# Optimization experiments

Hardware: AMD Instinct MI355X
Metric: run time of the kernel (lower is better)

The kernel has to match this reference:

```python
import jax, jax.numpy as jnp
import numpy as np

N = 50000        # num_nodes
E = 800000       # num edges (avg degree 16)
IN = 512         # embedding_dim[0]
H = 128          # hidden_dim = embedding_dim[1]
C = 64           # out_dim = n_classes = embedding_dim[-1]
L = 3            # layer_num = len(embedding_dim) - 1


def _lin(k, fan_in, fan_out):
    s = 1.0 / np.sqrt(fan_in)
    k1, k2 = jax.random.split(k)
    W = jax.random.uniform(k1, (fan_in, fan_out), jnp.float32, -s, s)
    b = jax.random.uniform(k2, (fan_out,), jnp.float32, -s, s)
    return W, b


def setup_inputs() -> dict:
    key = jax.random.key(0)
    ks = jax.random.split(key, 12)
    d = {}
    d["x"] = jax.random.normal(ks[0], (N, IN), jnp.float32)
    d["edge_index"] = jax.random.randint(ks[1], (2, E), 0, N)
    # pseudo_mlp: in_dim -> 512 -> 64 -> out_dim
    d["Wp1"], d["bp1"] = _lin(ks[2], IN, 512)
    d["Wp2"], d["bp2"] = _lin(ks[3], 512, 64)
    d["Wp3"], d["bp3"] = _lin(ks[4], 64, C)
    # parsing_mats[0] (only ln=0 is used in learn_soft_edge3), init ones/scaling_factor
    d["parsing0"] = jnp.ones((C, C), jnp.float32) / 2.0 + 0.01 * jax.random.normal(ks[5], (C, C), jnp.float32)
    # GCNConv weights (PyG style: linear without bias, bias added after aggregation)
    d["Wg0"], d["bg0"] = _lin(ks[6], IN, H)
    d["Wg1"], d["bg1"] = _lin(ks[7], H, H)
    d["Wg2"], d["bg2"] = _lin(ks[8], H, H)
    # JK 'cat' -> lin1 input is (layer_num-1)*hidden
    d["Wl1"], d["bl1"] = _lin(ks[9], (L - 1) * H, H)
    d["Wl2"], d["bl2"] = _lin(ks[10], H, C)
    return d


def gcn_conv(x, W, b, edge_index, ew, n):
    """PyG GCNConv with per-edge weight ew, add_self_loops=True (loop weight 1)."""
    xw = x @ W                                           # [N, F_out]
    row, col = edge_index[0], edge_index[1]
    loop = jnp.arange(n)
    row2 = jnp.concatenate([row, loop])
    col2 = jnp.concatenate([col, loop])
    ew2 = jnp.concatenate([ew, jnp.ones((n,), xw.dtype)])
    deg = jax.ops.segment_sum(ew2, col2, num_segments=n)
    dis = jnp.where(deg > 0, jax.lax.rsqrt(deg), 0.0)    # deg^-1/2, inf -> 0
    norm = dis[row2] * ew2 * dis[col2]                   # [E+N]
    out = jax.ops.segment_sum(norm[:, None] * xw[row2], col2, num_segments=n)
    return out + b


def soft_edge_weight(x, edge_index, Wp1, bp1, Wp2, bp2, Wp3, bp3, parsing0):
    """learn_soft_edge3: bilinear form start^T * relu(2*P) * end per edge.
    Original materializes an [E,C,C] outer product then bmm + diagonal; the
    diagonal-sum equals einsum('ek,ed,dk->e', start, end, parsing), computed
    here as a fused small matmul + elementwise reduce (same math)."""
    h = jax.nn.relu(x @ Wp1 + bp1)
    h = jax.nn.relu(h @ Wp2 + bp2)
    logits = h @ Wp3 + bp3                               # [N, C]
    parsing = jax.nn.relu(2.0 * parsing0)                # scaling_factor = 2
    s = logits[edge_index[0]]                            # [E, C] start
    e = logits[edge_index[1]]                            # [E, C] end
    ew = jnp.sum((e @ parsing) * s, axis=-1)             # [E]
    mean = ew.mean()
    var = jnp.var(ew, ddof=1)                            # torch .var() is unbiased
    return (ew - mean) * jnp.sqrt(1e-4 / var) + 1.0


def reference(x, edge_index, Wp1, bp1, Wp2, bp2, Wp3, bp3, parsing0,
              Wg0, bg0, Wg1, bg1, Wg2, bg2, Wl1, bl1, Wl2, bl2):
    n = x.shape[0]
    ew = soft_edge_weight(x, edge_index, Wp1, bp1, Wp2, bp2, Wp3, bp3, parsing0)
    # layer 0
    x1 = jax.nn.relu(gcn_conv(x, Wg0, bg0, edge_index, ew, n))
    xs = [x1]
    # ln = 1 (not last): conv -> relu -> (dropout off in eval) -> append
    x2 = jax.nn.relu(gcn_conv(x1, Wg1, bg1, edge_index, ew, n))
    xs.append(x2)
    # ln = 2 (last layer): computed in original but loop breaks before append;
    # jump(xs) overwrites x, so the last conv's output never reaches the output.
    xj = jnp.concatenate(xs, axis=-1)                    # JK 'cat' -> [N, (L-1)*H]
    out = jax.nn.relu(xj @ Wl1 + bl1)
    out = out @ Wl2 + bl2                                # [N, C]
    return out
```

## Files before the change

### kernel.cpp

```cpp
#include <hip/hip_runtime.h>
#include <hip/hip_bf16.h>
#include <cmath>
#include <cstring>

#define NNODES 50000
#define NEDGES 800000
#define IND    512
#define HD     128
#define CD     64

typedef __bf16 bf16x8 __attribute__((ext_vector_type(8)));
typedef float  f32x4  __attribute__((ext_vector_type(4)));
typedef const __attribute__((address_space(1))) unsigned int* gu32p;
typedef __attribute__((address_space(3))) unsigned int* lu32p;

static const size_t XJ_B   = 0;
static const size_t HID_B  = 25600000;
static const size_t H1_B   = 51200000;
static const size_t XW_B   = 102400000;
static const size_t H2_B   = 115200000;
static const size_t LG_B   = 121600000;
static const size_t PE_B   = 128000000;
static const size_t WT_B   = 134400000;
static const size_t CSRR_B = 135300000;
static const size_t EWC_B  = 138500000;
static const size_t CSRW_B = 141700000;
static const size_t CNT_B  = 144900000;
static const size_t S_B    = 145100000;
static const size_t ZERO_BYTES = 200016;
static const size_t RP_B   = 145100016;
static const size_t WOFF_B = 145300020;
static const size_t INCL_B = 145500020;
static const size_t BSUM_B = 145700020;
static const size_t ST_B   = 145701044;
static const size_t DIS_B  = 145701052;

static const size_t WP1T_O = 0;
static const size_t WG0T_O = 524288;
static const size_t WP2T_O = 655360;
static const size_t WP3T_O = 720896;
static const size_t W2T_O  = 729088;
static const size_t WG1T_O = 737280;
static const size_t WL1T_O = 770048;
static const size_t WL2T_O = 835584;
static const size_t BG1_O  = 851968;
static const size_t BG3_O  = 854528;

struct WD { const float* s; __hip_bfloat16* d; int K; int N; };
struct PrepArgs {
    const float* x; __hip_bfloat16* xb;
    WD w[7];
    int bo[8];
    const float* Wp3; const float* bp3; const float* P0; const float* bp1;
    __hip_bfloat16* W2t; float* bias_g1; float* bias_g3;
};
#define PREP_CAST_BLKS 12500
#define PREP_TP_BLKS   1648
#define PREP_BLKS      (PREP_CAST_BLKS + PREP_TP_BLKS + 20)

__global__ __launch_bounds__(256) void prep_all(PrepArgs a)
{
    int b = blockIdx.x;
    int t = threadIdx.x;
    if (b < PREP_CAST_BLKS) {
        int i = b * 256 + t;
        const float4* p = (const float4*)a.x + (size_t)i * 2;
        float4 u = p[0], v = p[1];
        __hip_bfloat16 o[8] __attribute__((aligned(16)));
        o[0] = __float2bfloat16(u.x); o[1] = __float2bfloat16(u.y);
        o[2] = __float2bfloat16(u.z); o[3] = __float2bfloat16(u.w);
        o[4] = __float2bfloat16(v.x); o[5] = __float2bfloat16(v.y);
        o[6] = __float2bfloat16(v.z); o[7] = __float2bfloat16(v.w);
        *(int4*)(a.xb + (size_t)i * 8) = *(const int4*)o;
        return;
    }
    b -= PREP_CAST_BLKS;
    if (b < PREP_TP_BLKS) {
        int m = 0;
        #pragma unroll
        for (int q = 1; q < 7; q++) if (b >= a.bo[q]) m = q;
        WD d = a.w[m];
        int i = (b - a.bo[m]) * 256 + t;
        if (i < d.K * d.N) {
            int k = i % d.K, n = i / d.K;
            d.d[i] = __float2bfloat16(d.s[(size_t)k * d.N + n]);
        }
        return;
    }
    b -= PREP_TP_BLKS;
    if (b < 16) {
        int i = b * 256 + t;
        int k = i >> 6, n = i & 63;
        float s = 0.f;
        for (int j = 0; j < 64; j++)
            s += a.Wp3[k * 64 + j] * fmaxf(2.f * a.P0[j * 64 + n], 0.f);
        a.W2t[n * 64 + k] = __float2bfloat16(s);
    } else if (b == 16) {
        int n = t;
        if (n < 64) {
            float s = 0.f;
            for (int j = 0; j < 64; j++)
                s += a.bp3[j] * fmaxf(2.f * a.P0[j * 64 + n], 0.f);
            a.bias_g3[n] = a.bp3[n];
            a.bias_g3[64 + n] = s;
        }
    } else {
        int i = (b - 17) * 256 + t;
        if (i < 512) a.bias_g1[i] = a.bp1[i];
        else if (i < 640) a.bias_g1[i] = 0.f;
    }
}

template<int BM, int BN, int WN>
__global__ __launch_bounds__(256) void gemm_mfma(
    const __hip_bfloat16* __restrict__ Ab, int lda,
    const __hip_bfloat16* __restrict__ Bt, int ldb,
    const float* __restrict__ bias,
    void* __restrict__ Cout, int ldc,
    void* __restrict__ Cout2, int ldc2, int splitN,
    int M, int K, int do_relu, int out_bf16)
{
    constexpr int BF = WN / 16;
    constexpr int MI = BM / 32;
    constexpr int APASS = BM / 64;
    constexpr int BPASS = BN / 64;
    __shared__ __bf16 As[2][BM * 32];
    __shared__ __bf16 Bs[2][BN * 32];

    const int NC = gridDim.x, NR = gridDim.y;
    int g = blockIdx.y * NC + blockIdx.x;
    int per = NC * 8;
    int nfull = (NR >> 3) * per;
    int rowt, colt;
    if (g < nfull) {
        int grp = g / per, rem = g % per;
        rowt = grp * 8 + (rem & 7);
        colt = rem >> 3;
    } else {
        int rem = g - nfull;
        int tail = NR - (NR >> 3) * 8;
        rowt = (NR >> 3) * 8 + rem % tail;
        colt = rem / tail;
    }

    const int t = threadIdx.x;
    const int row0 = rowt * BM;
    const int col0 = colt * BN;

    const int wv   = t >> 6;
    const int lane = t & 63;
    const int quad = lane >> 4;
    const int l16  = lane & 15;
    const int wrow = (wv >> 1) * (BM / 2);
    const int wcol = (wv & 1) * WN;

    const int subrow = lane >> 2;
    const int kchunk = (lane & 3) ^ (subrow & 3);
    const int subkg  = kchunk * 8;

    f32x4 acc[MI][BF] = {};

    for (int k0 = 0; k0 < K; k0 += 64) {
        #pragma unroll
        for (int h = 0; h < 2; h++) {
            int kh = k0 + h * 32;
            #pragma unroll
            for (int p = 0; p < APASS; p++) {
                int rowA = (p * 4 + wv) * 16 + subrow;
                const __hip_bfloat16* gp = Ab + (size_t)(row0 + rowA) * lda + kh + subkg;
                __builtin_amdgcn_global_load_lds((gu32p)(const void*)gp,
                    (lu32p)(void*)&As[h][(p * 4 + wv) * 512], 16, 0, 0);
            }
            #pragma unroll
            for (int p = 0; p < BPASS; p++) {
                int rowB = (p * 4 + wv) * 16 + subrow;
                const __hip_bfloat16* gp = Bt + (size_t)(col0 + rowB) * ldb + kh + subkg;
                __builtin_amdgcn_global_load_lds((gu32p)(const void*)gp,
                    (lu32p)(void*)&Bs[h][(p * 4 + wv) * 512], 16, 0, 0);
            }
        }
        __syncthreads();

        #pragma unroll
        for (int h = 0; h < 2; h++) {
            bf16x8 af[MI], bfr[BF];
            #pragma unroll
            for (int i = 0; i < MI; i++) {
                int R = wrow + i * 16 + l16;
                af[i] = *(const bf16x8*)&As[h][R * 32 + ((quad ^ (R & 3)) * 8)];
            }
            #pragma unroll
            for (int j = 0; j < BF; j++) {
                int R = wcol + j * 16 + l16;
                bfr[j] = *(const bf16x8*)&Bs[h][R * 32 + ((quad ^ (R & 3)) * 8)];
            }
            #pragma unroll
            for (int i = 0; i < MI; i++)
                #pragma unroll
                for (int j = 0; j < BF; j++)
                    acc[i][j] = __builtin_amdgcn_mfma_f32_16x16x32_bf16(af[i], bfr[j], acc[i][j], 0, 0, 0);
        }
        if (k0 + 64 < K) __syncthreads();
    }

    #pragma unroll
    for (int i = 0; i < MI; i++) {
        #pragma unroll
        for (int j = 0; j < BF; j++) {
            int n = col0 + wcol + j * 16 + l16;
            bool second = (n >= splitN);
            float bv = bias ? bias[n] : 0.f;
            #pragma unroll
            for (int reg = 0; reg < 4; reg++) {
                int m = row0 + wrow + i * 16 + quad * 4 + reg;
                if (m >= M) continue;
                float v = acc[i][j][reg] + bv;
                if (do_relu && !second) v = fmaxf(v, 0.f);
                if (second)
                    ((__hip_bfloat16*)Cout2)[(size_t)m * ldc2 + (n - splitN)] = __float2bfloat16(v);
                else if (out_bf16)
                    ((__hip_bfloat16*)Cout)[(size_t)m * ldc + n] = __float2bfloat16(v);
                else
                    ((float*)Cout)[(size_t)m * ldc + n] = v;
            }
        }
    }
}

__global__ __launch_bounds__(256) void count_kernel(
    const int* __restrict__ ei, int* __restrict__ cnt)
{
    int e = blockIdx.x * 256 + threadIdx.x;
    if (e >= NEDGES) return;
    atomicAdd(&cnt[ei[NEDGES + e]], 1);
}

__global__ __launch_bounds__(256) void scan1_kernel(
    const int* __restrict__ cnt, int* __restrict__ incl, int* __restrict__ bsum)
{
    __shared__ int s[256];
    int t = threadIdx.x;
    int i = blockIdx.x * 256 + t;
    int v = (i < NNODES) ? cnt[i] : 0;
    s[t] = v;
    __syncthreads();
    for (int off = 1; off < 256; off <<= 1) {
        int u = (t >= off) ? s[t - off] : 0;
        __syncthreads();
        s[t] += u;
        __syncthreads();
    }
    if (i < NNODES) incl[i] = s[t];
    if (t == 255) bsum[blockIdx.x] = s[255];
}

__global__ __launch_bounds__(256) void scan3_kernel(
    const int* __restrict__ cnt, const int* __restrict__ incl,
    const int* __restrict__ bsum, int* __restrict__ rowptr,
    int* __restrict__ woff, int nb)
{
    __shared__ int s[256];
    int t = threadIdx.x;
    int v = (t < nb) ? bsum[t] : 0;
    s[t] = v;
    __syncthreads();
    for (int off = 1; off < 256; off <<= 1) {
        int u = (t >= off) ? s[t - off] : 0;
        __syncthreads();
        s[t] += u;
        __syncthreads();
    }
    int off = s[blockIdx.x] - bsum[blockIdx.x];
    int i = blockIdx.x * 256 + t;
    if (i >= NNODES) return;
    int r = incl[i] - cnt[i] + off;
    rowptr[i] = r;
    woff[i] = r;
    if (i == NNODES - 1) rowptr[NNODES] = incl[i] + off;
}

__global__ __launch_bounds__(256) void scatter_idx_kernel(
    const int* __restrict__ ei, int* __restrict__ woff,
    int* __restrict__ csr_row, int* __restrict__ csr_col)
{
    int e = blockIdx.x * 256 + threadIdx.x;
    if (e >= NEDGES) return;
    int r = ei[e];
    int c = ei[NEDGES + e];
    int p = atomicAdd(&woff[c], 1);
    csr_row[p] = r;
    csr_col[p] = c;
}

__global__ __launch_bounds__(256) void edge_ew_gather(
    const __hip_bfloat16* __restrict__ lg, const __hip_bfloat16* __restrict__ pe,
    const int* __restrict__ csr_row, const int* __restrict__ csr_col,
    float* __restrict__ ew_csr)
{
    const int tid = threadIdx.x;
    const int sub = tid & 7;
    const int e = blockIdx.x * 32 + (tid >> 3);
    if (e >= NEDGES) return;
    int r = csr_row[e];
    int c = csr_col[e];
    bf16x8 a = *(const bf16x8*)(lg + (size_t)r * CD + sub * 8);
    bf16x8 b = *(const bf16x8*)(pe + (size_t)c * CD + sub * 8);
    float acc = 0.f;
    #pragma unroll
    for (int u = 0; u < 8; u++)
        acc += (float)a[u] * (float)b[u];
    acc += __shfl_xor(acc, 1);
    acc += __shfl_xor(acc, 2);
    acc += __shfl_xor(acc, 4);
    if (sub == 0) ew_csr[e] = acc;
}

__global__ __launch_bounds__(256) void ew_stats_kernel(
    const float* __restrict__ ew, double* __restrict__ S)
{
    const int tid = threadIdx.x;
    double s1 = 0.0, s2 = 0.0;
    for (int i = blockIdx.x * 256 + tid; i < NEDGES; i += gridDim.x * 256) {
        float v = ew[i];
        s1 += v; s2 += (double)v * (double)v;
    }
    __shared__ double sh1[256], sh2[256];
    sh1[tid] = s1; sh2[tid] = s2;
    __syncthreads();
    for (int s = 128; s > 0; s >>= 1) {
        if (tid < s) { sh1[tid] += sh1[tid + s]; sh2[tid] += sh2[tid + s]; }
        __syncthreads();
    }
    if (tid == 0) {
        atomicAdd(&S[0], sh1[0]);
        atomicAdd(&S[1], sh2[0]);
    }
}

__global__ __launch_bounds__(256) void norm_deg_kernel(
    const int* __restrict__ rowptr, float* __restrict__ ew_csr,
    const double* __restrict__ S, float* __restrict__ dis)
{
    int n = blockIdx.x * 256 + threadIdx.x;
    if (n >= NNODES) return;
    const double Ed = (double)NEDGES;
    double meand = S[0] / Ed;
    double var = (S[1] - S[0] * S[0] / Ed) / (Ed - 1.0);
    float mean = (float)meand;
    float alpha = (float)sqrt(1e-4 / var);
    int s = rowptr[n], e = rowptr[n + 1];
    float sum = 0.f;
    for (int j = s; j < e; j++) {
        float w = (ew_csr[j] - mean) * alpha + 1.0f;
        ew_csr[j] = w;
        sum += w;
    }
    float d = sum + 1.0f;
    dis[n] = (d > 0.f) ? rsqrtf(d) : 0.f;
}

__global__ __launch_bounds__(256) void csrw_kernel(
    const int* __restrict__ rowptr, const int* __restrict__ csr_row,
    const float* __restrict__ ew_csr, const float* __restrict__ dis,
    float* __restrict__ csr_w)
{
    int n = blockIdx.x * 256 + threadIdx.x;
    if (n >= NNODES) return;
    float dn = dis[n];
    int s = rowptr[n], e = rowptr[n + 1];
    for (int j = s; j < e; j++)
        csr_w[j] = dis[csr_row[j]] * ew_csr[j] * dn;
}

__global__ __launch_bounds__(128) void agg_kernel(
    const unsigned* __restrict__ xw32, const float* __restrict__ dis,
    const int* __restrict__ rowptr, const int* __restrict__ csr_row,
    const float* __restrict__ csr_w, const float* __restrict__ bias,
    __hip_bfloat16* __restrict__ out, int ldo)
{
    const int wv = threadIdx.x >> 6, lane = threadIdx.x & 63;
    const int n = blockIdx.x * 2 + wv;
    if (n >= NNODES) return;
    float dn = dis[n];
    unsigned v0 = xw32[(size_t)n * 64 + lane];
    float aL = dn * dn * __uint_as_float(v0 << 16);
    float aH = dn * dn * __uint_as_float(v0 & 0xffff0000u);
    int s = rowptr[n], e = rowptr[n + 1];
    int j = s;
    for (; j + 4 <= e; j += 4) {
        int r0 = csr_row[j], r1 = csr_row[j + 1];
        int r2 = csr_row[j + 2], r3 = csr_row[j + 3];
        float w0 = csr_w[j], w1 = csr_w[j + 1];
        float w2 = csr_w[j + 2], w3 = csr_w[j + 3];
        unsigned g0 = xw32[(size_t)r0 * 64 + lane];
        unsigned g1 = xw32[(size_t)r1 * 64 + lane];
        unsigned g2 = xw32[(size_t)r2 * 64 + lane];
        unsigned g3 = xw32[(size_t)r3 * 64 + lane];
        aL = fmaf(w0, __uint_as_float(g0 << 16), aL);
        aH = fmaf(w0, __uint_as_float(g0 & 0xffff0000u), aH);
        aL = fmaf(w1, __uint_as_float(g1 << 16), aL);
        aH = fmaf(w1, __uint_as_float(g1 & 0xffff0000u), aH);
        aL = fmaf(w2, __uint_as_float(g2 << 16), aL);
        aH = fmaf(w2, __uint_as_float(g2 & 0xffff0000u), aH);
        aL = fmaf(w3, __uint_as_float(g3 << 16), aL);
        aH = fmaf(w3, __uint_as_float(g3 & 0xffff0000u), aH);
    }
    for (; j < e; j++) {
        int r = csr_row[j];
        float w = csr_w[j];
        unsigned g = xw32[(size_t)r * 64 + lane];
        aL = fmaf(w, __uint_as_float(g << 16), aL);
        aH = fmaf(w, __uint_as_float(g & 0xffff0000u), aH);
    }
    float2 b = *(const float2*)(bias + 2 * lane);
    aL = fmaxf(aL + b.x, 0.f);
    aH = fmaxf(aH + b.y, 0.f);
    __hip_bfloat16 bl = __float2bfloat16(aL), bh = __float2bfloat16(aH);
    unsigned short ul, uh;
    memcpy(&ul, &bl, 2); memcpy(&uh, &bh, 2);
    unsigned o = (unsigned)ul | ((unsigned)uh << 16);
    *(unsigned*)(out + (size_t)n * ldo + 2 * lane) = o;
}

extern "C" void kernel_launch(void* const* d_in, const int* in_sizes, int n_in,
                              void* d_out, int out_size, void* d_ws, size_t ws_size,
                              hipStream_t stream)
{
    const float* x   = (const float*)d_in[0];
    const int*   ei  = (const int*)d_in[1];
    const float* Wp1 = (const float*)d_in[2];
    const float* bp1 = (const float*)d_in[3];
    const float* Wp2 = (const float*)d_in[4];
    const float* bp2 = (const float*)d_in[5];
    const float* Wp3 = (const float*)d_in[6];
    const float* bp3 = (const float*)d_in[7];
    const float* P0  = (const float*)d_in[8];
    const float* Wg0 = (const float*)d_in[9];
    const float* bg0 = (const float*)d_in[10];
    const float* Wg1 = (const float*)d_in[11];
    const float* bg1 = (const float*)d_in[12];
    const float* Wl1 = (const float*)d_in[15];
    const float* bl1 = (const float*)d_in[16];
    const float* Wl2 = (const float*)d_in[17];
    const float* bl2 = (const float*)d_in[18];
    float* out = (float*)d_out;

    char* wsb = (char*)d_ws;
    __hip_bfloat16* xj     = (__hip_bfloat16*)(wsb + XJ_B);
    __hip_bfloat16* xb16   = (__hip_bfloat16*)(wsb + XJ_B);
    __hip_bfloat16* hid    = (__hip_bfloat16*)(wsb + HID_B);
    __hip_bfloat16* h1     = (__hip_bfloat16*)(wsb + H1_B);
    __hip_bfloat16* xw     = (__hip_bfloat16*)(wsb + XW_B);
    __hip_bfloat16* h2     = (__hip_bfloat16*)(wsb + H2_B);
    __hip_bfloat16* lg     = (__hip_bfloat16*)(wsb + LG_B);
    __hip_bfloat16* pe     = (__hip_bfloat16*)(wsb + PE_B);
    int*            csr_row= (int*)(wsb + CSRR_B);
    float*          ew_csr = (float*)(wsb + EWC_B);
    int*            csr_col= (int*)(wsb + CSRW_B);
    float*          csr_w  = (float*)(wsb + CSRW_B);
    int*            cnt    = (int*)(wsb + CNT_B);
    double*         S      = (double*)(wsb + S_B);
    int*            rowptr = (int*)(wsb + RP_B);
    int*            woff   = (int*)(wsb + WOFF_B);
    int*            incl   = (int*)(wsb + INCL_B);
    int*            bsum   = (int*)(wsb + BSUM_B);
    float*          dis    = (float*)(wsb + DIS_B);

    __hip_bfloat16* Wp1t = (__hip_bfloat16*)(wsb + WT_B + WP1T_O);
    __hip_bfloat16* Wg0t = (__hip_bfloat16*)(wsb + WT_B + WG0T_O);
    __hip_bfloat16* Wp2t = (__hip_bfloat16*)(wsb + WT_B + WP2T_O);
    __hip_bfloat16* Wp3t = (__hip_bfloat16*)(wsb + WT_B + WP3T_O);
    __hip_bfloat16* W2t  = (__hip_bfloat16*)(wsb + WT_B + W2T_O);
    __hip_bfloat16* Wg1t = (__hip_bfloat16*)(wsb + WT_B + WG1T_O);
    __hip_bfloat16* Wl1t = (__hip_bfloat16*)(wsb + WT_B + WL1T_O);
    __hip_bfloat16* Wl2t = (__hip_bfloat16*)(wsb + WT_B + WL2T_O);
    float*          bias_g1 = (float*)(wsb + WT_B + BG1_O);
    float*          bias_g3 = (float*)(wsb + WT_B + BG3_O);

    const int EB = (NEDGES + 255) / 256;
    const int NB = (NNODES + 255) / 256;
    const int MT  = (NNODES + 127) / 128;
    const int MT64 = (NNODES + 63) / 64;
    const int BIGN = 1 << 30;

    hipMemsetAsync(wsb + CNT_B, 0, ZERO_BYTES, stream);

    PrepArgs pa;
    pa.x = x; pa.xb = xb16;
    pa.w[0] = { Wp1, Wp1t, 512, 512 };
    pa.w[1] = { Wg0, Wg0t, 512, 128 };
    pa.w[2] = { Wp2, Wp2t, 512,  64 };
    pa.w[3] = { Wp3, Wp3t,  64,  64 };
    pa.w[4] = { Wg1, Wg1t, 128, 128 };
    pa.w[5] = { Wl1, Wl1t, 256, 128 };
    pa.w[6] = { Wl2, Wl2t, 128,  64 };
    pa.bo[0] = 0;    pa.bo[1] = 1024; pa.bo[2] = 1280; pa.bo[3] = 1408;
    pa.bo[4] = 1424; pa.bo[5] = 1488; pa.bo[6] = 1616; pa.bo[7] = 1648;
    pa.Wp3 = Wp3; pa.bp3 = bp3; pa.P0 = P0; pa.bp1 = bp1;
    pa.W2t = W2t; pa.bias_g1 = bias_g1; pa.bias_g3 = bias_g3;
    prep_all<<<PREP_BLKS, 256, 0, stream>>>(pa);

    count_kernel<<<EB, 256, 0, stream>>>(ei, cnt);
    scan1_kernel<<<NB, 256, 0, stream>>>(cnt, incl, bsum);
    scan3_kernel<<<NB, 256, 0, stream>>>(cnt, incl, bsum, rowptr, woff, NB);
    scatter_idx_kernel<<<EB, 256, 0, stream>>>(ei, woff, csr_row, csr_col);

    gemm_mfma<128, 128, 64><<<dim3(5, MT), 256, 0, stream>>>(
        xb16, 512, Wp1t, 512, bias_g1, h1, 512, xw, 128, 512, NNODES, 512, 1, 1);

    gemm_mfma<64, 64, 32><<<dim3(1, MT64), 256, 0, stream>>>(
        h1, 512, Wp2t, 512, bp2, h2, 64, nullptr, 0, BIGN, NNODES, 512, 1, 1);

    gemm_mfma<64, 128, 64><<<dim3(1, MT64), 256, 0, stream>>>(
        h2, 64, Wp3t, 64, bias_g3, lg, 64, pe, 64, 64, NNODES, 64, 0, 1);

    edge_ew_gather<<<(NEDGES + 31) / 32, 256, 0, stream>>>(lg, pe, csr_row, csr_col, ew_csr);
    ew_stats_kernel<<<512, 256, 0, stream>>>(ew_csr, S);
    norm_deg_kernel<<<NB, 256, 0, stream>>>(rowptr, ew_csr, S, dis);
    csrw_kernel<<<NB, 256, 0, stream>>>(rowptr, csr_row, ew_csr, dis, csr_w);

    agg_kernel<<<25000, 128, 0, stream>>>((const unsigned*)xw, dis, rowptr, csr_row, csr_w, bg0, xj, 2 * HD);

    gemm_mfma<64, 64, 32><<<dim3(2, MT64), 256, 0, stream>>>(
        xj, 2 * HD, Wg1t, 128, nullptr, xw, 128, nullptr, 0, BIGN, NNODES, 128, 0, 1);
    agg_kernel<<<25000, 128, 0, stream>>>((const unsigned*)xw, dis, rowptr, csr_row, csr_w, bg1, xj + HD, 2 * HD);

    gemm_mfma<64, 64, 32><<<dim3(2, MT64), 256, 0, stream>>>(
        xj, 2 * HD, Wl1t, 256, bl1, hid, 128, nullptr, 0, BIGN, NNODES, 256, 1, 1);
    gemm_mfma<64, 64, 32><<<dim3(1, MT64), 256, 0, stream>>>(
        hid, 128, Wl2t, 128, bl2, out, 64, nullptr, 0, BIGN, NNODES, 128, 0, 0);
}
```

Before: 535.8 us.

## Fuse back-to-back MLP GEMM pairs into single kernel keeping hidden tile in LDS

Adds a gemm_fused kernel that computes a first GEMM with bias+ReLU, writes the bf16 result tile into shared memory, then multiplies it by a second weight matrix preloaded into LDS. This replaces the Wp2→Wp3 pseudo-MLP pair and the lin1→lin2 output head pair. It removes two kernel launches and the global-memory round trip of the intermediate h2/hid tensors. In exchange it uses more LDS per block, which may lower occupancy, and the second GEMM runs serially after the first within each block.

```diff
diff --git a/kernel.cpp b/kernel.cpp
--- a/kernel.cpp
+++ b/kernel.cpp
@@ -225,6 +225,156 @@
             }
         }
     }
+}
+
+template<int BN1, int WN1, int N2, int SPLIT2, int OUT2F32>
+__global__ __launch_bounds__(256) void gemm_fused(
+    const __hip_bfloat16* __restrict__ Ab, int lda,
+    const __hip_bfloat16* __restrict__ B1t, int ldb1,
+    const float* __restrict__ bias1,
+    const __hip_bfloat16* __restrict__ B2t,
+    const float* __restrict__ bias2,
+    void* __restrict__ Out1, int ldo1,
+    void* __restrict__ Out2, int ldo2,
+    int M, int K1)
+{
+    constexpr int BF1 = WN1 / 16;
+    constexpr int BPASS1 = BN1 / 64;
+    constexpr int K2H = BN1 / 32;
+    constexpr int WN2 = N2 / 2;
+    constexpr int BF2 = WN2 / 16;
+    constexpr int P2 = N2 / 64;
+    __shared__ __bf16 L1[4096 + BN1 * 64];
+    __shared__ __bf16 Bs2[8192];
+
+    const int t = threadIdx.x;
+    const int row0 = blockIdx.y * 64;
+    const int wv   = t >> 6;
+    const int lane = t & 63;
+    const int quad = lane >> 4;
+    const int l16  = lane & 15;
+    const int wrow1 = (wv >> 1) * 32;
+    const int wcol1 = (wv & 1) * WN1;
+    const int subrow = lane >> 2;
+    const int subkg  = ((lane & 3) ^ (subrow & 3)) * 8;
+
+    #pragma unroll
+    for (int hh = 0; hh < K2H; hh++)
+        #pragma unroll
+        for (int p = 0; p < P2; p++) {
+            int rowB = (p * 4 + wv) * 16 + subrow;
+            const __hip_bfloat16* gp = B2t + (size_t)rowB * BN1 + hh * 32 + subkg;
+            __builtin_amdgcn_global_load_lds((gu32p)(const void*)gp,
+                (lu32p)(void*)&Bs2[hh * (N2 * 32) + (p * 4 + wv) * 512], 16, 0, 0);
+        }
+
+    f32x4 acc1[2][BF1] = {};
+    for (int k0 = 0; k0 < K1; k0 += 64) {
+        #pragma unroll
+        for (int h = 0; h < 2; h++) {
+            int kh = k0 + h * 32;
+            {
+                int rowA = wv * 16 + subrow;
+                const __hip_bfloat16* gp = Ab + (size_t)(row0 + rowA) * lda + kh + subkg;
+                __builtin_amdgcn_global_load_lds((gu32p)(const void*)gp,
+                    (lu32p)(void*)&L1[h * 2048 + wv * 512], 16, 0, 0);
+            }
+            #pragma unroll
+            for (int p = 0; p < BPASS1; p++) {
+                int rowB = (p * 4 + wv) * 16 + subrow;
+                const __hip_bfloat16* gp = B1t + (size_t)rowB * ldb1 + kh + subkg;
+                __builtin_amdgcn_global_load_lds((gu32p)(const void*)gp,
+                    (lu32p)(void*)&L1[4096 + h * (BN1 * 32) + (p * 4 + wv) * 512], 16, 0, 0);
+            }
+        }
+        __syncthreads();
+        #pragma unroll
+        for (int h = 0; h < 2; h++) {
+            bf16x8 af[2], bfr[BF1];
+            #pragma unroll
+            for (int i = 0; i < 2; i++) {
+                int R = wrow1 + i * 16 + l16;
+                af[i] = *(const bf16x8*)&L1[h * 2048 + R * 32 + ((quad ^ (R & 3)) * 8)];
+            }
+            #pragma unroll
+            for (int j = 0; j < BF1; j++) {
+                int R = wcol1 + j * 16 + l16;
+                bfr[j] = *(const bf16x8*)&L1[4096 + h * (BN1 * 32) + R * 32 + ((quad ^ (R & 3)) * 8)];
+            }
+            #pragma unroll
+            for (int i = 0; i < 2; i++)
+                #pragma unroll
+                for (int j = 0; j < BF1; j++)
+                    acc1[i][j] = __builtin_amdgcn_mfma_f32_16x16x32_bf16(af[i], bfr[j], acc1[i][j], 0, 0, 0);
+        }
+        __syncthreads();
+    }
+
+    #pragma unroll
+    for (int i = 0; i < 2; i++)
+        #pragma unroll
+        for (int j = 0; j < BF1; j++) {
+            int n1 = wcol1 + j * 16 + l16;
+            float bv = bias1[n1];
+            int h = n1 >> 5, kk = n1 & 31;
+            int q = kk >> 3, pp = kk & 7;
+            #pragma unroll
+            for (int reg = 0; reg < 4; reg++) {
+                int r = wrow1 + i * 16 + quad * 4 + reg;
+                float v = fmaxf(acc1[i][j][reg] + bv, 0.f);
+                __hip_bfloat16 hb = __float2bfloat16(v);
+                unsigned short us; memcpy(&us, &hb, 2);
+                *(unsigned short*)&L1[h * 2048 + r * 32 + ((q ^ (r & 3)) * 8) + pp] = us;
+            }
+        }
+    __syncthreads();
+
+    const int wrow2 = (wv >> 1) * 32;
+    const int wcol2 = (wv & 1) * WN2;
+    f32x4 acc2[2][BF2] = {};
+    #pragma unroll
+    for (int hh = 0; hh < K2H; hh++) {
+        bf16x8 af2[2], bf2[BF2];
+        #pragma unroll
+        for (int i = 0; i < 2; i++) {
+            int R = wrow2 + i * 16 + l16;
+            af2[i] = *(const bf16x8*)&L1[hh * 2048 + R * 32 + ((quad ^ (R & 3)) * 8)];
+        }
+        #pragma unroll
+        for (int j = 0; j < BF2; j++) {
+            int R = wcol2 + j * 16 + l16;
+            bf2[j] = *(const bf16x8*)&Bs2[hh * (N2 * 32) + R * 32 + ((quad ^ (R & 3)) * 8)];
+        }
+        #pragma unroll
+        for (int i = 0; i < 2; i++)
+            #pragma unroll
+            for (int j = 0; j < BF2; j++)
+                acc2[i][j] = __builtin_amdgcn_mfma_f32_16x16x32_bf16(af2[i], bf2[j], acc2[i][j], 0, 0, 0);
+    }
+
+    #pragma unroll
+    for (int i = 0; i < 2; i++)
+        #pragma unroll
+        for (int j = 0; j < BF2; j++) {
+            int n2 = wcol2 + j * 16 + l16;
+            float bv = bias2[n2];
+            #pragma unroll
+            for (int reg = 0; reg < 4; reg++) {
+                int m = row0 + wrow2 + i * 16 + quad * 4 + reg;
+                if (m >= M) continue;
+                float v = acc2[i][j][reg] + bv;
+                if (SPLIT2) {
+                    if (n2 < 64)
+                        ((__hip_bfloat16*)Out1)[(size_t)m * ldo1 + n2] = __float2bfloat16(v);
+                    else
+                        ((__hip_bfloat16*)Out2)[(size_t)m * ldo2 + (n2 - 64)] = __float2bfloat16(v);
+                } else if (OUT2F32) {
+                    ((float*)Out1)[(size_t)m * ldo1 + n2] = v;
+                } else {
+                    ((__hip_bfloat16*)Out1)[(size_t)m * ldo1 + n2] = __float2bfloat16(v);
+                }
+            }
+        }
 }
 
 __global__ __launch_bounds__(256) void count_kernel(
@@ -448,10 +598,8 @@
     char* wsb = (char*)d_ws;
     __hip_bfloat16* xj     = (__hip_bfloat16*)(wsb + XJ_B);
     __hip_bfloat16* xb16   = (__hip_bfloat16*)(wsb + XJ_B);
-    __hip_bfloat16* hid    = (__hip_bfloat16*)(wsb + HID_B);
     __hip_bfloat16* h1     = (__hip_bfloat16*)(wsb + H1_B);
     __hip_bfloat16* xw     = (__hip_bfloat16*)(wsb + XW_B);
-    __hip_bfloat16* h2     = (__hip_bfloat16*)(wsb + H2_B);
     __hip_bfloat16* lg     = (__hip_bfloat16*)(wsb + LG_B);
     __hip_bfloat16* pe     = (__hip_bfloat16*)(wsb + PE_B);
     int*            csr_row= (int*)(wsb + CSRR_B);
@@ -508,11 +656,8 @@
     gemm_mfma<128, 128, 64><<<dim3(5, MT), 256, 0, stream>>>(
         xb16, 512, Wp1t, 512, bias_g1, h1, 512, xw, 128, 512, NNODES, 512, 1, 1);
 
-    gemm_mfma<64, 64, 32><<<dim3(1, MT64), 256, 0, stream>>>(
-        h1, 512, Wp2t, 512, bp2, h2, 64, nullptr, 0, BIGN, NNODES, 512, 1, 1);
-
-    gemm_mfma<64, 128, 64><<<dim3(1, MT64), 256, 0, stream>>>(
-        h2, 64, Wp3t, 64, bias_g3, lg, 64, pe, 64, 64, NNODES, 64, 0, 1);
+    gemm_fused<64, 32, 128, 1, 0><<<dim3(1, MT64), 256, 0, stream>>>(
+        h1, 512, Wp2t, 512, bp2, Wp3t, bias_g3, lg, 64, pe, 64, NNODES, 512);
 
     edge_ew_gather<<<(NEDGES + 31) / 32, 256, 0, stream>>>(lg, pe, csr_row, csr_col, ew_csr);
     ew_stats_kernel<<<512, 256, 0, stream>>>(ew_csr, S);
@@ -525,8 +670,6 @@
         xj, 2 * HD, Wg1t, 128, nullptr, xw, 128, nullptr, 0, BIGN, NNODES, 128, 0, 1);
     agg_kernel<<<25000, 128, 0, stream>>>((const unsigned*)xw, dis, rowptr, csr_row, csr_w, bg1, xj + HD, 2 * HD);
 
-    gemm_mfma<64, 64, 32><<<dim3(2, MT64), 256, 0, stream>>>(
-        xj, 2 * HD, Wl1t, 256, bl1, hid, 128, nullptr, 0, BIGN, NNODES, 256, 1, 1);
-    gemm_mfma<64, 64, 32><<<dim3(1, MT64), 256, 0, stream>>>(
-        hid, 128, Wl2t, 128, bl2, out, 64, nullptr, 0, BIGN, NNODES, 128, 0, 0);
-}
+    gemm_fused<128, 64, 64, 0, 1><<<dim3(1, MT64), 256, 0, stream>>>(
+        xj, 2 * HD, Wl1t, 256, bl1, Wl2t, bl2, out, 64, nullptr, 0, NNODES, 256);
+}
```

Result: faster. 523.2 us (-2.3%).
